# Optimization experiments

Measured on AMD Instinct MI355X. Metric: run time of the kernel, lower is better.

The kernel has to match this reference:

```python
import jax, jax.numpy as jnp
import numpy as np

JITTER_EPS = 0.01  # router_jitter_noise


def sparsemixer_top2(scores, jitter_eps):
    # scores: [T, E]. Faithful port of PhiMoE sparsemixer (top_k == 2).
    E = scores.shape[-1]
    eye = jnp.arange(E)
    # ---- expert 1 ----
    max1 = jnp.max(scores, axis=-1, keepdims=True)
    ind1 = jnp.argmax(scores, axis=-1)                      # [T]
    factor1 = jnp.maximum(jnp.abs(scores), max1)            # scores.abs().clamp(min=max)
    mask1 = (max1 - scores) / factor1 > 2.0 * jitter_eps
    gates1 = jax.nn.softmax(jnp.where(mask1, -jnp.inf, scores), axis=-1)
    mult1 = jnp.take_along_axis(gates1, ind1[:, None], axis=-1)   # [T,1]
    # ---- expert 2: mask out first pick, repeat ----
    oh1 = eye[None, :] == ind1[:, None]
    masked_scores = jnp.where(oh1, -jnp.inf, scores)
    max2 = jnp.max(masked_scores, axis=-1, keepdims=True)
    ind2 = jnp.argmax(masked_scores, axis=-1)
    factor2 = jnp.maximum(jnp.abs(scores), max2)
    mask2 = (max2 - scores) / factor2 > 2.0 * jitter_eps
    gates2 = jax.nn.softmax(jnp.where(mask2, -jnp.inf, masked_scores), axis=-1)
    mult2 = jnp.take_along_axis(gates2, ind2[:, None], axis=-1)   # [T,1]
    topk_w = jnp.concatenate([mult1, mult2], axis=-1)       # [T,2]
    topk_ids = jnp.stack([ind1, ind2], axis=-1)             # [T,2]
    return topk_w, topk_ids


def setup_inputs() -> dict:
    key = jax.random.key(0)
    ks = jax.random.split(key, 5)
    B, S, D, F, E = 2, 2048, 1024, 2048, 8
    hidden_states = jax.random.normal(ks[0], (B, S, D), dtype=jnp.float32)
    gate_w = jax.random.normal(ks[1], (E, D), dtype=jnp.float32) * (D ** -0.5)
    w_gate = jax.random.normal(ks[2], (E, F, D), dtype=jnp.float32) * (D ** -0.5)
    w_up = jax.random.normal(ks[3], (E, F, D), dtype=jnp.float32) * (D ** -0.5)
    w_down = jax.random.normal(ks[4], (E, D, F), dtype=jnp.float32) * (F ** -0.5)
    return {"hidden_states": hidden_states, "gate_w": gate_w,
            "w_gate": w_gate, "w_up": w_up, "w_down": w_down}


def reference(hidden_states, gate_w, w_gate, w_up, w_down):
    B, S, D = hidden_states.shape
    E = gate_w.shape[0]
    x = hidden_states.reshape(-1, D)                         # [T,D]
    router_logits = x @ gate_w.T                             # [T,E]
    topk_w, topk_ids = sparsemixer_top2(router_logits, JITTER_EPS)
    # per-token combine weights over experts: [T,E]
    comb = jnp.sum(topk_w[:, :, None] *
                   (topk_ids[:, :, None] == jnp.arange(E)[None, None, :]).astype(topk_w.dtype),
                   axis=1)
    out = jnp.zeros_like(x)
    for e in range(E):  # small fixed expert count
        h = jax.nn.silu(x @ w_gate[e].T) * (x @ w_up[e].T)   # [T,F]
        out = out + comb[:, e:e + 1] * (h @ w_down[e].T)     # [T,D]
    return out.reshape(B, S, D), router_logits
```

## Files before the change

### kernel.cpp

```cpp
#include <hip/hip_runtime.h>
#include <stdint.h>

#define TOK    4096
#define DMODEL 1024
#define FDIM   2048
#define NEXP   8
#define MAXP   9216
#define MAXT   72
#define OUT_MAIN (TOK * DMODEL)

#define IDX_CNT 0
#define IDX_CUR 8
#define IDX_SEG 16
#define IDX_NT  24
#define IDX_TE  32
#define IDX_TR  112

#define OFF_META 0
#define OFF_TKE  1024
#define OFF_TKW  33792
#define OFF_PTOK 66560
#define OFF_PW   103424
#define OFF_XG   140288
#define OFF_H    19014656
#define OFF_WGB  56763392
#define OFF_WUB  90317824
#define OFF_WDB  123872256
#define WS_NEED  157426688

typedef __attribute__((ext_vector_type(8))) __bf16 bf16x8;
typedef __attribute__((ext_vector_type(8))) unsigned short u16x8;
typedef __attribute__((ext_vector_type(4))) unsigned short u16x4;
typedef __attribute__((ext_vector_type(4))) float f32x4;

__device__ __forceinline__ unsigned short f2bf(float f) {
  unsigned u = __builtin_bit_cast(unsigned, f);
  u += 0x7fffu + ((u >> 16) & 1u);
  return (unsigned short)(u >> 16);
}

__device__ __forceinline__ void async_load16(const void* g, void* l) {
  __builtin_amdgcn_global_load_lds(
      (__attribute__((address_space(1))) void*)g,
      (__attribute__((address_space(3))) void*)l, 16, 0, 0);
}

__device__ __forceinline__ bf16x8 ld_frag(const unsigned short* p) {
  return __builtin_bit_cast(bf16x8, *(const u16x8*)p);
}

__device__ __forceinline__ f32x4 zero4() { f32x4 z = {0.f, 0.f, 0.f, 0.f}; return z; }

__global__ void k_conv(const float* __restrict__ src, unsigned short* __restrict__ dst) {
  size_t i = ((size_t)blockIdx.x * 256 + threadIdx.x) * 8;
  float4 a = *(const float4*)(src + i);
  float4 b = *(const float4*)(src + i + 4);
  u16x8 v = {f2bf(a.x), f2bf(a.y), f2bf(a.z), f2bf(a.w),
             f2bf(b.x), f2bf(b.y), f2bf(b.z), f2bf(b.w)};
  *(u16x8*)(dst + i) = v;
}

__global__ void k_router(const float* __restrict__ x, const float* __restrict__ gw,
                         float* __restrict__ logits) {
  int lane = threadIdx.x & 63;
  int t = blockIdx.x * 4 + (threadIdx.x >> 6);
  double acc[NEXP];
#pragma unroll
  for (int e = 0; e < NEXP; ++e) acc[e] = 0.0;
  const float* xp = x + (size_t)t * DMODEL;
  for (int i = 0; i < DMODEL / 64; ++i) {
    int d = i * 64 + lane;
    float xv = xp[d];
#pragma unroll
    for (int e = 0; e < NEXP; ++e) acc[e] += (double)xv * (double)gw[e * DMODEL + d];
  }
#pragma unroll
  for (int e = 0; e < NEXP; ++e) {
    double v = acc[e];
#pragma unroll
    for (int off = 32; off > 0; off >>= 1) v += __shfl_down(v, off, 64);
    if (lane == 0) logits[t * NEXP + e] = (float)v;
  }
}

__global__ void k_routing(const float* __restrict__ logits, int* __restrict__ meta,
                          int* __restrict__ tk_e, float* __restrict__ tk_w) {
  int t = blockIdx.x * blockDim.x + threadIdx.x;
  float s[NEXP];
#pragma unroll
  for (int e = 0; e < NEXP; ++e) s[e] = logits[t * NEXP + e];
  float max1 = s[0]; int ind1 = 0;
#pragma unroll
  for (int e = 1; e < NEXP; ++e) if (s[e] > max1) { max1 = s[e]; ind1 = e; }
  float sum1 = 0.f;
#pragma unroll
  for (int e = 0; e < NEXP; ++e) {
    float f = fmaxf(fabsf(s[e]), max1);
    if (!((max1 - s[e]) / f > 0.02f)) sum1 += expf(s[e] - max1);
  }
  float w1 = 1.f / sum1;
  float max2 = -3.4e38f; int ind2 = 0;
#pragma unroll
  for (int e = 0; e < NEXP; ++e) if (e != ind1 && s[e] > max2) { max2 = s[e]; ind2 = e; }
  float sum2 = 0.f;
#pragma unroll
  for (int e = 0; e < NEXP; ++e) {
    if (e == ind1) continue;
    float f = fmaxf(fabsf(s[e]), max2);
    if (!((max2 - s[e]) / f > 0.02f)) sum2 += expf(s[e] - max2);
  }
  float w2 = 1.f / sum2;
  tk_e[2 * t] = ind1; tk_e[2 * t + 1] = ind2;
  tk_w[2 * t] = w1;   tk_w[2 * t + 1] = w2;
  atomicAdd(&meta[IDX_CNT + ind1], 1);
  atomicAdd(&meta[IDX_CNT + ind2], 1);
}

__global__ void k_scan(int* __restrict__ meta) {
  if (threadIdx.x != 0) return;
  int off = 0, nt = 0;
  for (int e = 0; e < NEXP; ++e) {
    meta[IDX_SEG + e] = off;
    int cnt = meta[IDX_CNT + e];
    int tiles = (cnt + 127) >> 7;
    for (int j = 0; j < tiles; ++j) {
      meta[IDX_TE + nt] = e;
      meta[IDX_TR + nt] = off + (j << 7);
      ++nt;
    }
    off += tiles << 7;
  }
  meta[IDX_NT] = nt;
}

__global__ void k_scatter(const int* __restrict__ tk_e, const float* __restrict__ tk_w,
                          int* __restrict__ meta, int* __restrict__ ptok,
                          float* __restrict__ pw) {
  int t = blockIdx.x * blockDim.x + threadIdx.x;
#pragma unroll
  for (int k = 0; k < 2; ++k) {
    int e = tk_e[2 * t + k];
    int p = atomicAdd(&meta[IDX_CUR + e], 1);
    int r = meta[IDX_SEG + e] + p;
    ptok[r] = t;
    pw[r] = tk_w[2 * t + k];
  }
}

__global__ void k_gather(const float* __restrict__ x, const int* __restrict__ ptok,
                         unsigned short* __restrict__ xg) {
  int r = blockIdx.x;
  int t = ptok[r];
  int c = threadIdx.x << 2;
  unsigned short o0 = 0, o1 = 0, o2 = 0, o3 = 0;
  if (t >= 0) {
    float4 v = *(const float4*)(x + ((size_t)t << 10) + c);
    o0 = f2bf(v.x); o1 = f2bf(v.y); o2 = f2bf(v.z); o3 = f2bf(v.w);
  }
  u16x4 o = {o0, o1, o2, o3};
  *(u16x4*)(xg + ((size_t)r << 10) + c) = o;
}

template <bool PRE>
__global__ __launch_bounds__(256, 3) void k_gu(
    const unsigned short* __restrict__ xg,
    const float* __restrict__ w_gate32, const float* __restrict__ w_up32,
    const unsigned short* __restrict__ w_gateb, const unsigned short* __restrict__ w_upb,
    unsigned short* __restrict__ h, const int* __restrict__ meta) {
  int nt = meta[IDX_NT];
  int rt = blockIdx.y;
  if (rt >= nt) return;
  int e = meta[IDX_TE + rt];
  int row0 = meta[IDX_TR + rt];
  int n0 = blockIdx.x * 128;

  __shared__ __align__(16) unsigned short As[8192], Bg[8192], Bu[8192];

  int tid = threadIdx.x;
  int lane = tid & 63;
  int w = tid >> 6;
  int wm = w >> 1, wn = w & 1;
  int fr = lane & 15, fq = lane >> 4;

  f32x4 accg[16], accu[16];
#pragma unroll
  for (int i = 0; i < 16; ++i) { accg[i] = zero4(); accu[i] = zero4(); }

  for (int ks = 0; ks < DMODEL / 64; ++ks) {
    int k0 = ks * 64;
    if (ks) __syncthreads();
#pragma unroll
    for (int i = 0; i < 4; ++i) {
      int c = w * 4 + i;
      int msub = c >> 1, ksub = c & 1;
      const unsigned short* gp =
          xg + (size_t)(row0 + msub * 16 + fr) * DMODEL + (k0 + ksub * 32 + fq * 8);
      async_load16(gp, &As[c * 512]);
    }
    if constexpr (PRE) {
      const unsigned short* Wg = w_gateb + (size_t)e * FDIM * DMODEL;
      const unsigned short* Wu = w_upb + (size_t)e * FDIM * DMODEL;
#pragma unroll
      for (int i = 0; i < 4; ++i) {
        int c = w * 4 + i;
        int nrow = n0 + ((c >> 1) << 4) + fr;
        int kk = k0 + ((c & 1) << 5) + (fq << 3);
        size_t off = (size_t)nrow * DMODEL + kk;
        async_load16(Wg + off, &Bg[c * 512]);
        async_load16(Wu + off, &Bu[c * 512]);
      }
    } else {
      const float* Wg = w_gate32 + (size_t)e * FDIM * DMODEL;
      const float* Wu = w_up32 + (size_t)e * FDIM * DMODEL;
#pragma unroll
      for (int i = 0; i < 4; ++i) {
        int tau = tid + 256 * i;
        int c = tau >> 6, l = tau & 63;
        int nrow = n0 + ((c >> 1) << 4) + (l & 15);
        int kk = k0 + ((c & 1) << 5) + ((l >> 4) << 3);
        const float* sg = Wg + (size_t)nrow * DMODEL + kk;
        const float* su = Wu + (size_t)nrow * DMODEL + kk;
        float4 g0 = *(const float4*)sg;
        float4 g1 = *(const float4*)(sg + 4);
        float4 u0 = *(const float4*)su;
        float4 u1 = *(const float4*)(su + 4);
        u16x8 vg = {f2bf(g0.x), f2bf(g0.y), f2bf(g0.z), f2bf(g0.w),
                    f2bf(g1.x), f2bf(g1.y), f2bf(g1.z), f2bf(g1.w)};
        u16x8 vu = {f2bf(u0.x), f2bf(u0.y), f2bf(u0.z), f2bf(u0.w),
                    f2bf(u1.x), f2bf(u1.y), f2bf(u1.z), f2bf(u1.w)};
        *(u16x8*)&Bg[c * 512 + l * 8] = vg;
        *(u16x8*)&Bu[c * 512 + l * 8] = vu;
      }
    }
    __syncthreads();
#pragma unroll
    for (int ksub = 0; ksub < 2; ++ksub) {
      bf16x8 a[4];
#pragma unroll
      for (int ms = 0; ms < 4; ++ms)
        a[ms] = ld_frag(&As[(((wm * 4 + ms) << 1) + ksub) * 512 + lane * 8]);
#pragma unroll
      for (int ns = 0; ns < 4; ++ns) {
        bf16x8 vg = ld_frag(&Bg[(((wn * 4 + ns) << 1) + ksub) * 512 + lane * 8]);
        bf16x8 vu = ld_frag(&Bu[(((wn * 4 + ns) << 1) + ksub) * 512 + lane * 8]);
#pragma unroll
        for (int ms = 0; ms < 4; ++ms) {
          accg[ms * 4 + ns] =
              __builtin_amdgcn_mfma_f32_16x16x32_bf16(a[ms], vg, accg[ms * 4 + ns], 0, 0, 0);
          accu[ms * 4 + ns] =
              __builtin_amdgcn_mfma_f32_16x16x32_bf16(a[ms], vu, accu[ms * 4 + ns], 0, 0, 0);
        }
      }
    }
  }
#pragma unroll
  for (int ms = 0; ms < 4; ++ms) {
#pragma unroll
    for (int ns = 0; ns < 4; ++ns) {
      f32x4 g4 = accg[ms * 4 + ns], u4 = accu[ms * 4 + ns];
#pragma unroll
      for (int i = 0; i < 4; ++i) {
        int lrow = wm * 64 + ms * 16 + fq * 4 + i;
        int col = n0 + wn * 64 + ns * 16 + fr;
        float gv = g4[i], uv = u4[i];
        float hv = gv * uv / (1.f + __expf(-gv));
        h[(size_t)(row0 + lrow) * FDIM + col] = f2bf(hv);
      }
    }
  }
}

template <bool PRE>
__global__ __launch_bounds__(256, 3) void k_down(
    const unsigned short* __restrict__ h, const float* __restrict__ w_down32,
    const unsigned short* __restrict__ w_downb, float* __restrict__ out,
    const int* __restrict__ meta, const int* __restrict__ ptok,
    const float* __restrict__ pw) {
  int nt = meta[IDX_NT];
  int rt = blockIdx.y;
  if (rt >= nt) return;
  int e = meta[IDX_TE + rt];
  int row0 = meta[IDX_TR + rt];
  int d0 = blockIdx.x * 128;

  __shared__ __align__(16) unsigned short Ah[8192], Bd[8192];
  __shared__ int stok[128];
  __shared__ float sw[128];

  int tid = threadIdx.x;
  int lane = tid & 63;
  int w = tid >> 6;
  int wm = w >> 1, wn = w & 1;
  int fr = lane & 15, fq = lane >> 4;

  if (tid < 128) { stok[tid] = ptok[row0 + tid]; sw[tid] = pw[row0 + tid]; }

  f32x4 acc[16];
#pragma unroll
  for (int i = 0; i < 16; ++i) acc[i] = zero4();

  for (int ks = 0; ks < FDIM / 64; ++ks) {
    int k0 = ks * 64;
    if (ks) __syncthreads();
#pragma unroll
    for (int i = 0; i < 4; ++i) {
      int c = w * 4 + i;
      int msub = c >> 1, ksub = c & 1;
      const unsigned short* gp =
          h + (size_t)(row0 + msub * 16 + fr) * FDIM + (k0 + ksub * 32 + fq * 8);
      async_load16(gp, &Ah[c * 512]);
    }
    if constexpr (PRE) {
      const unsigned short* Wd = w_downb + (size_t)e * DMODEL * FDIM;
#pragma unroll
      for (int i = 0; i < 4; ++i) {
        int c = w * 4 + i;
        int drow = d0 + ((c >> 1) << 4) + fr;
        int kk = k0 + ((c & 1) << 5) + (fq << 3);
        async_load16(Wd + (size_t)drow * FDIM + kk, &Bd[c * 512]);
      }
    } else {
      const float* Wd = w_down32 + (size_t)e * DMODEL * FDIM;
#pragma unroll
      for (int i = 0; i < 4; ++i) {
        int tau = tid + 256 * i;
        int c = tau >> 6, l = tau & 63;
        int drow = d0 + ((c >> 1) << 4) + (l & 15);
        int kk = k0 + ((c & 1) << 5) + ((l >> 4) << 3);
        const float* sd = Wd + (size_t)drow * FDIM + kk;
        float4 b0 = *(const float4*)sd;
        float4 b1 = *(const float4*)(sd + 4);
        u16x8 vb = {f2bf(b0.x), f2bf(b0.y), f2bf(b0.z), f2bf(b0.w),
                    f2bf(b1.x), f2bf(b1.y), f2bf(b1.z), f2bf(b1.w)};
        *(u16x8*)&Bd[c * 512 + l * 8] = vb;
      }
    }
    __syncthreads();
#pragma unroll
    for (int ksub = 0; ksub < 2; ++ksub) {
      bf16x8 a[4];
#pragma unroll
      for (int ms = 0; ms < 4; ++ms)
        a[ms] = ld_frag(&Ah[(((wm * 4 + ms) << 1) + ksub) * 512 + lane * 8]);
#pragma unroll
      for (int ns = 0; ns < 4; ++ns) {
        bf16x8 vb = ld_frag(&Bd[(((wn * 4 + ns) << 1) + ksub) * 512 + lane * 8]);
#pragma unroll
        for (int ms = 0; ms < 4; ++ms)
          acc[ms * 4 + ns] =
              __builtin_amdgcn_mfma_f32_16x16x32_bf16(a[ms], vb, acc[ms * 4 + ns], 0, 0, 0);
      }
    }
  }
#pragma unroll
  for (int ms = 0; ms < 4; ++ms) {
#pragma unroll
    for (int ns = 0; ns < 4; ++ns) {
      f32x4 v4 = acc[ms * 4 + ns];
#pragma unroll
      for (int i = 0; i < 4; ++i) {
        int lrow = wm * 64 + ms * 16 + fq * 4 + i;
        int col = d0 + wn * 64 + ns * 16 + fr;
        int t = stok[lrow];
        if (t >= 0) atomicAdd(&out[(size_t)t * DMODEL + col], v4[i] * sw[lrow]);
      }
    }
  }
}

extern "C" void kernel_launch(void* const* d_in, const int* in_sizes, int n_in,
                              void* d_out, int out_size, void* d_ws, size_t ws_size,
                              hipStream_t stream) {
  const float* x  = (const float*)d_in[0];
  const float* gw = (const float*)d_in[1];
  const float* wg = (const float*)d_in[2];
  const float* wu = (const float*)d_in[3];
  const float* wd = (const float*)d_in[4];
  float* out = (float*)d_out;
  float* logits = out + OUT_MAIN;

  char* wsb = (char*)d_ws;
  int* meta = (int*)(wsb + OFF_META);
  int* tk_e = (int*)(wsb + OFF_TKE);
  float* tk_w = (float*)(wsb + OFF_TKW);
  int* ptok = (int*)(wsb + OFF_PTOK);
  float* pw = (float*)(wsb + OFF_PW);
  unsigned short* xg = (unsigned short*)(wsb + OFF_XG);
  unsigned short* h = (unsigned short*)(wsb + OFF_H);
  unsigned short* wgb = (unsigned short*)(wsb + OFF_WGB);
  unsigned short* wub = (unsigned short*)(wsb + OFF_WUB);
  unsigned short* wdb = (unsigned short*)(wsb + OFF_WDB);

  bool pre = ws_size >= (size_t)WS_NEED;

  hipMemsetAsync(out, 0, (size_t)OUT_MAIN * sizeof(float), stream);
  hipMemsetAsync(meta, 0, 64, stream);
  hipMemsetAsync(ptok, 0xFF, MAXP * sizeof(int), stream);
  hipMemsetAsync(pw, 0, MAXP * sizeof(float), stream);

  if (pre) {
    k_conv<<<8192, 256, 0, stream>>>(wg, wgb);
    k_conv<<<8192, 256, 0, stream>>>(wu, wub);
    k_conv<<<8192, 256, 0, stream>>>(wd, wdb);
  }

  k_router<<<TOK / 4, 256, 0, stream>>>(x, gw, logits);
  k_routing<<<TOK / 256, 256, 0, stream>>>(logits, meta, tk_e, tk_w);
  k_scan<<<1, 64, 0, stream>>>(meta);
  k_scatter<<<TOK / 256, 256, 0, stream>>>(tk_e, tk_w, meta, ptok, pw);
  k_gather<<<MAXP, 256, 0, stream>>>(x, ptok, xg);
  if (pre) {
    k_gu<true><<<dim3(FDIM / 128, MAXT), 256, 0, stream>>>(xg, wg, wu, wgb, wub, h, meta);
    k_down<true><<<dim3(DMODEL / 128, MAXT), 256, 0, stream>>>(h, wd, wdb, out, meta, ptok, pw);
  } else {
    k_gu<false><<<dim3(FDIM / 128, MAXT), 256, 0, stream>>>(xg, wg, wu, wgb, wub, h, meta);
    k_down<false><<<dim3(DMODEL / 128, MAXT), 256, 0, stream>>>(h, wd, wdb, out, meta, ptok, pw);
  }
}
```

Before: 623.6 us.

## Replace atomic scatter-add with per-row stores plus combine kernel, halve N tiles

The down-projection now writes each routed row's result to a workspace buffer that reuses the gate-weight bf16 region. A new combine kernel then computes each token's output as the weighted sum of its two expert rows, using positions recorded during scatter. This removes the float atomicAdds and the memset of the output buffer. Both GEMM kernels also shrink their N tile from 128 to 64, which doubles the block count and halves accumulator registers, and k_down's occupancy hint rises to 4. The cost is an extra intermediate write and read, less reuse of the A tile per block, and a larger workspace requirement that decides whether this path is taken.

```diff
diff --git a/kernel.cpp b/kernel.cpp
--- a/kernel.cpp
+++ b/kernel.cpp
@@ -26,7 +26,9 @@
 #define OFF_WGB  56763392
 #define OFF_WUB  90317824
 #define OFF_WDB  123872256
-#define WS_NEED  157426688
+#define OFF_PV   OFF_WGB
+#define OFF_RPOS 157426688
+#define WS_NEED  157459456
 
 typedef __attribute__((ext_vector_type(8))) __bf16 bf16x8;
 typedef __attribute__((ext_vector_type(8))) unsigned short u16x8;
@@ -135,7 +137,7 @@
 
 __global__ void k_scatter(const int* __restrict__ tk_e, const float* __restrict__ tk_w,
                           int* __restrict__ meta, int* __restrict__ ptok,
-                          float* __restrict__ pw) {
+                          float* __restrict__ pw, int* __restrict__ rpos) {
   int t = blockIdx.x * blockDim.x + threadIdx.x;
 #pragma unroll
   for (int k = 0; k < 2; ++k) {
@@ -144,6 +146,7 @@
     int r = meta[IDX_SEG + e] + p;
     ptok[r] = t;
     pw[r] = tk_w[2 * t + k];
+    rpos[2 * t + k] = r;
   }
 }
 
@@ -172,19 +175,19 @@
   if (rt >= nt) return;
   int e = meta[IDX_TE + rt];
   int row0 = meta[IDX_TR + rt];
-  int n0 = blockIdx.x * 128;
-
-  __shared__ __align__(16) unsigned short As[8192], Bg[8192], Bu[8192];
+  int n0 = blockIdx.x * 64;
+
+  __shared__ __align__(16) unsigned short As[8192], Bg[4096], Bu[4096];
 
   int tid = threadIdx.x;
   int lane = tid & 63;
   int w = tid >> 6;
-  int wm = w >> 1, wn = w & 1;
+  int wm = w & 1, wn = w >> 1;
   int fr = lane & 15, fq = lane >> 4;
 
-  f32x4 accg[16], accu[16];
-#pragma unroll
-  for (int i = 0; i < 16; ++i) { accg[i] = zero4(); accu[i] = zero4(); }
+  f32x4 accg[8], accu[8];
+#pragma unroll
+  for (int i = 0; i < 8; ++i) { accg[i] = zero4(); accu[i] = zero4(); }
 
   for (int ks = 0; ks < DMODEL / 64; ++ks) {
     int k0 = ks * 64;
@@ -201,8 +204,8 @@
       const unsigned short* Wg = w_gateb + (size_t)e * FDIM * DMODEL;
       const unsigned short* Wu = w_upb + (size_t)e * FDIM * DMODEL;
 #pragma unroll
-      for (int i = 0; i < 4; ++i) {
-        int c = w * 4 + i;
+      for (int i = 0; i < 2; ++i) {
+        int c = w * 2 + i;
         int nrow = n0 + ((c >> 1) << 4) + fr;
         int kk = k0 + ((c & 1) << 5) + (fq << 3);
         size_t off = (size_t)nrow * DMODEL + kk;
@@ -213,7 +216,7 @@
       const float* Wg = w_gate32 + (size_t)e * FDIM * DMODEL;
       const float* Wu = w_up32 + (size_t)e * FDIM * DMODEL;
 #pragma unroll
-      for (int i = 0; i < 4; ++i) {
+      for (int i = 0; i < 2; ++i) {
         int tau = tid + 256 * i;
         int c = tau >> 6, l = tau & 63;
         int nrow = n0 + ((c >> 1) << 4) + (l & 15);
@@ -240,15 +243,15 @@
       for (int ms = 0; ms < 4; ++ms)
         a[ms] = ld_frag(&As[(((wm * 4 + ms) << 1) + ksub) * 512 + lane * 8]);
 #pragma unroll
-      for (int ns = 0; ns < 4; ++ns) {
-        bf16x8 vg = ld_frag(&Bg[(((wn * 4 + ns) << 1) + ksub) * 512 + lane * 8]);
-        bf16x8 vu = ld_frag(&Bu[(((wn * 4 + ns) << 1) + ksub) * 512 + lane * 8]);
+      for (int ns = 0; ns < 2; ++ns) {
+        bf16x8 vg = ld_frag(&Bg[(((wn * 2 + ns) << 1) + ksub) * 512 + lane * 8]);
+        bf16x8 vu = ld_frag(&Bu[(((wn * 2 + ns) << 1) + ksub) * 512 + lane * 8]);
 #pragma unroll
         for (int ms = 0; ms < 4; ++ms) {
-          accg[ms * 4 + ns] =
-              __builtin_amdgcn_mfma_f32_16x16x32_bf16(a[ms], vg, accg[ms * 4 + ns], 0, 0, 0);
-          accu[ms * 4 + ns] =
-              __builtin_amdgcn_mfma_f32_16x16x32_bf16(a[ms], vu, accu[ms * 4 + ns], 0, 0, 0);
+          accg[ms * 2 + ns] =
+              __builtin_amdgcn_mfma_f32_16x16x32_bf16(a[ms], vg, accg[ms * 2 + ns], 0, 0, 0);
+          accu[ms * 2 + ns] =
+              __builtin_amdgcn_mfma_f32_16x16x32_bf16(a[ms], vu, accu[ms * 2 + ns], 0, 0, 0);
         }
       }
     }
@@ -256,12 +259,12 @@
 #pragma unroll
   for (int ms = 0; ms < 4; ++ms) {
 #pragma unroll
-    for (int ns = 0; ns < 4; ++ns) {
-      f32x4 g4 = accg[ms * 4 + ns], u4 = accu[ms * 4 + ns];
+    for (int ns = 0; ns < 2; ++ns) {
+      f32x4 g4 = accg[ms * 2 + ns], u4 = accu[ms * 2 + ns];
 #pragma unroll
       for (int i = 0; i < 4; ++i) {
         int lrow = wm * 64 + ms * 16 + fq * 4 + i;
-        int col = n0 + wn * 64 + ns * 16 + fr;
+        int col = n0 + wn * 32 + ns * 16 + fr;
         float gv = g4[i], uv = u4[i];
         float hv = gv * uv / (1.f + __expf(-gv));
         h[(size_t)(row0 + lrow) * FDIM + col] = f2bf(hv);
@@ -271,33 +274,35 @@
 }
 
 template <bool PRE>
-__global__ __launch_bounds__(256, 3) void k_down(
+__global__ __launch_bounds__(256, 4) void k_down(
     const unsigned short* __restrict__ h, const float* __restrict__ w_down32,
     const unsigned short* __restrict__ w_downb, float* __restrict__ out,
-    const int* __restrict__ meta, const int* __restrict__ ptok,
-    const float* __restrict__ pw) {
+    float* __restrict__ pv, const int* __restrict__ meta,
+    const int* __restrict__ ptok, const float* __restrict__ pw) {
   int nt = meta[IDX_NT];
   int rt = blockIdx.y;
   if (rt >= nt) return;
   int e = meta[IDX_TE + rt];
   int row0 = meta[IDX_TR + rt];
-  int d0 = blockIdx.x * 128;
-
-  __shared__ __align__(16) unsigned short Ah[8192], Bd[8192];
+  int d0 = blockIdx.x * 64;
+
+  __shared__ __align__(16) unsigned short Ah[8192], Bd[4096];
   __shared__ int stok[128];
   __shared__ float sw[128];
 
   int tid = threadIdx.x;
   int lane = tid & 63;
   int w = tid >> 6;
-  int wm = w >> 1, wn = w & 1;
+  int wm = w & 1, wn = w >> 1;
   int fr = lane & 15, fq = lane >> 4;
 
-  if (tid < 128) { stok[tid] = ptok[row0 + tid]; sw[tid] = pw[row0 + tid]; }
-
-  f32x4 acc[16];
-#pragma unroll
-  for (int i = 0; i < 16; ++i) acc[i] = zero4();
+  if constexpr (!PRE) {
+    if (tid < 128) { stok[tid] = ptok[row0 + tid]; sw[tid] = pw[row0 + tid]; }
+  }
+
+  f32x4 acc[8];
+#pragma unroll
+  for (int i = 0; i < 8; ++i) acc[i] = zero4();
 
   for (int ks = 0; ks < FDIM / 64; ++ks) {
     int k0 = ks * 64;
@@ -313,8 +318,8 @@
     if constexpr (PRE) {
       const unsigned short* Wd = w_downb + (size_t)e * DMODEL * FDIM;
 #pragma unroll
-      for (int i = 0; i < 4; ++i) {
-        int c = w * 4 + i;
+      for (int i = 0; i < 2; ++i) {
+        int c = w * 2 + i;
         int drow = d0 + ((c >> 1) << 4) + fr;
         int kk = k0 + ((c & 1) << 5) + (fq << 3);
         async_load16(Wd + (size_t)drow * FDIM + kk, &Bd[c * 512]);
@@ -322,7 +327,7 @@
     } else {
       const float* Wd = w_down32 + (size_t)e * DMODEL * FDIM;
 #pragma unroll
-      for (int i = 0; i < 4; ++i) {
+      for (int i = 0; i < 2; ++i) {
         int tau = tid + 256 * i;
         int c = tau >> 6, l = tau & 63;
         int drow = d0 + ((c >> 1) << 4) + (l & 15);
@@ -343,29 +348,49 @@
       for (int ms = 0; ms < 4; ++ms)
         a[ms] = ld_frag(&Ah[(((wm * 4 + ms) << 1) + ksub) * 512 + lane * 8]);
 #pragma unroll
-      for (int ns = 0; ns < 4; ++ns) {
-        bf16x8 vb = ld_frag(&Bd[(((wn * 4 + ns) << 1) + ksub) * 512 + lane * 8]);
+      for (int ns = 0; ns < 2; ++ns) {
+        bf16x8 vb = ld_frag(&Bd[(((wn * 2 + ns) << 1) + ksub) * 512 + lane * 8]);
 #pragma unroll
         for (int ms = 0; ms < 4; ++ms)
-          acc[ms * 4 + ns] =
-              __builtin_amdgcn_mfma_f32_16x16x32_bf16(a[ms], vb, acc[ms * 4 + ns], 0, 0, 0);
+          acc[ms * 2 + ns] =
+              __builtin_amdgcn_mfma_f32_16x16x32_bf16(a[ms], vb, acc[ms * 2 + ns], 0, 0, 0);
       }
     }
   }
 #pragma unroll
   for (int ms = 0; ms < 4; ++ms) {
 #pragma unroll
-    for (int ns = 0; ns < 4; ++ns) {
-      f32x4 v4 = acc[ms * 4 + ns];
+    for (int ns = 0; ns < 2; ++ns) {
+      f32x4 v4 = acc[ms * 2 + ns];
 #pragma unroll
       for (int i = 0; i < 4; ++i) {
         int lrow = wm * 64 + ms * 16 + fq * 4 + i;
-        int col = d0 + wn * 64 + ns * 16 + fr;
-        int t = stok[lrow];
-        if (t >= 0) atomicAdd(&out[(size_t)t * DMODEL + col], v4[i] * sw[lrow]);
-      }
-    }
-  }
+        int col = d0 + wn * 32 + ns * 16 + fr;
+        if constexpr (PRE) {
+          pv[(size_t)(row0 + lrow) * DMODEL + col] = v4[i];
+        } else {
+          int t = stok[lrow];
+          if (t >= 0) atomicAdd(&out[(size_t)t * DMODEL + col], v4[i] * sw[lrow]);
+        }
+      }
+    }
+  }
+}
+
+__global__ void k_combine(const float* __restrict__ pv, const int* __restrict__ rpos,
+                          const float* __restrict__ tkw, float* __restrict__ out) {
+  int t = blockIdx.x;
+  int r1 = rpos[2 * t], r2 = rpos[2 * t + 1];
+  float w1 = tkw[2 * t], w2 = tkw[2 * t + 1];
+  int c = threadIdx.x << 2;
+  float4 a = *(const float4*)(pv + (size_t)r1 * DMODEL + c);
+  float4 b = *(const float4*)(pv + (size_t)r2 * DMODEL + c);
+  float4 o;
+  o.x = w1 * a.x + w2 * b.x;
+  o.y = w1 * a.y + w2 * b.y;
+  o.z = w1 * a.z + w2 * b.z;
+  o.w = w1 * a.w + w2 * b.w;
+  *(float4*)(out + (size_t)t * DMODEL + c) = o;
 }
 
 extern "C" void kernel_launch(void* const* d_in, const int* in_sizes, int n_in,
@@ -390,13 +415,17 @@
   unsigned short* wgb = (unsigned short*)(wsb + OFF_WGB);
   unsigned short* wub = (unsigned short*)(wsb + OFF_WUB);
   unsigned short* wdb = (unsigned short*)(wsb + OFF_WDB);
+  float* pv = (float*)(wsb + OFF_PV);
+  int* rpos = (int*)(wsb + OFF_RPOS);
 
   bool pre = ws_size >= (size_t)WS_NEED;
 
-  hipMemsetAsync(out, 0, (size_t)OUT_MAIN * sizeof(float), stream);
   hipMemsetAsync(meta, 0, 64, stream);
   hipMemsetAsync(ptok, 0xFF, MAXP * sizeof(int), stream);
-  hipMemsetAsync(pw, 0, MAXP * sizeof(float), stream);
+  if (!pre) {
+    hipMemsetAsync(out, 0, (size_t)OUT_MAIN * sizeof(float), stream);
+    hipMemsetAsync(pw, 0, MAXP * sizeof(float), stream);
+  }
 
   if (pre) {
     k_conv<<<8192, 256, 0, stream>>>(wg, wgb);
@@ -407,13 +436,14 @@
   k_router<<<TOK / 4, 256, 0, stream>>>(x, gw, logits);
   k_routing<<<TOK / 256, 256, 0, stream>>>(logits, meta, tk_e, tk_w);
   k_scan<<<1, 64, 0, stream>>>(meta);
-  k_scatter<<<TOK / 256, 256, 0, stream>>>(tk_e, tk_w, meta, ptok, pw);
+  k_scatter<<<TOK / 256, 256, 0, stream>>>(tk_e, tk_w, meta, ptok, pw, rpos);
   k_gather<<<MAXP, 256, 0, stream>>>(x, ptok, xg);
   if (pre) {
-    k_gu<true><<<dim3(FDIM / 128, MAXT), 256, 0, stream>>>(xg, wg, wu, wgb, wub, h, meta);
-    k_down<true><<<dim3(DMODEL / 128, MAXT), 256, 0, stream>>>(h, wd, wdb, out, meta, ptok, pw);
+    k_gu<true><<<dim3(FDIM / 64, MAXT), 256, 0, stream>>>(xg, wg, wu, wgb, wub, h, meta);
+    k_down<true><<<dim3(DMODEL / 64, MAXT), 256, 0, stream>>>(h, wd, wdb, out, pv, meta, ptok, pw);
+    k_combine<<<TOK, 256, 0, stream>>>(pv, rpos, tk_w, out);
   } else {
-    k_gu<false><<<dim3(FDIM / 128, MAXT), 256, 0, stream>>>(xg, wg, wu, wgb, wub, h, meta);
-    k_down<false><<<dim3(DMODEL / 128, MAXT), 256, 0, stream>>>(h, wd, wdb, out, meta, ptok, pw);
-  }
-}
+    k_gu<false><<<dim3(FDIM / 64, MAXT), 256, 0, stream>>>(xg, wg, wu, wgb, wub, h, meta);
+    k_down<false><<<dim3(DMODEL / 64, MAXT), 256, 0, stream>>>(h, wd, wdb, out, pv, meta, ptok, pw);
+  }
+}
```

Measured after the change: 590.7 us. 5.3% less time.
